# Performance work log

Measured on AMD Instinct MI355X. Metric: run time of the kernel, lower is better.

The kernel has to match this reference:

```python
import jax, jax.numpy as jnp
import numpy as np

T, B, F, H = 2048, 50, 750, 100  # time, batch(seen by LSTM), input feat, hidden
OUT = 2

def setup_inputs() -> dict:
    key = jax.random.key(0)
    ks = jax.random.split(key, 7)
    s = 1.0 / np.sqrt(H)
    u = lambda k, shape: jax.random.uniform(k, shape, jnp.float32, -s, s)
    return {
        "x": jax.random.normal(ks[0], (T, B, F), jnp.float32),
        "W_ih": u(ks[1], (4 * H, F)),
        "W_hh": u(ks[2], (4 * H, H)),
        "b_ih": u(ks[3], (4 * H,)),
        "b_hh": u(ks[4], (4 * H,)),
        "fc_W": u(ks[5], (OUT, B * H)),
        "fc_b": u(ks[6], (OUT,)),
    }

def reference(x, W_ih, W_hh, b_ih, b_hh, fc_W, fc_b):
    # PyTorch LSTM (batch_first=False): scan over dim0. Gate order: i, f, g, o.
    # Precompute input projections for all steps at once: (T, B, 4H)
    x_proj = jnp.einsum('tbf,gf->tbg', x, W_ih) + b_ih + b_hh

    def step(carry, xp):
        h, c = carry                      # (B, H) each
        gates = xp + h @ W_hh.T           # (B, 4H)
        i, f, g, o = jnp.split(gates, 4, axis=-1)
        i = jax.nn.sigmoid(i)
        f = jax.nn.sigmoid(f)
        g = jnp.tanh(g)
        o = jax.nn.sigmoid(o)
        c = f * c + i * g
        h = o * jnp.tanh(c)
        return (h, c), h

    h0 = jnp.zeros((B, H), x.dtype)
    c0 = jnp.zeros((B, H), x.dtype)
    _, hs = jax.lax.scan(step, (h0, c0), x_proj)  # hs: (T, B, H)
    flat = hs.reshape(hs.shape[0], -1)            # (T, B*H) == (T, 5000)
    return flat @ fc_W.T + fc_b                   # (T, 2)
```

## Files before the change

kernel.cpp:

```cpp
#include <hip/hip_runtime.h>

#define T_DIM 2048
#define B_DIM 50
#define F_DIM 750
#define H_DIM 100
#define G4    400
#define M_DIM (T_DIM * B_DIM)
#define KPAD  768

typedef __attribute__((ext_vector_type(8))) short short8v;
typedef __attribute__((ext_vector_type(4))) float f32x4;

__device__ __forceinline__ float fast_rcp(float x) { return __builtin_amdgcn_rcpf(x); }
__device__ __forceinline__ float sigm_f(float x) {
    return fast_rcp(1.0f + __expf(-x));
}
__device__ __forceinline__ float tanh_f(float x) {
    return 1.0f - 2.0f * fast_rcp(__expf(2.0f * x) + 1.0f);
}

__device__ __forceinline__ unsigned short f2bf(float f) {
    unsigned int u = __float_as_uint(f);
    u = (u + 0x7FFFu + ((u >> 16) & 1u)) >> 16;
    return (unsigned short)u;
}
__device__ __forceinline__ float bf2f(unsigned short h) {
    return __uint_as_float(((unsigned int)h) << 16);
}

template <int CTRL>
__device__ __forceinline__ float qperm(float x) {
    return __int_as_float(__builtin_amdgcn_mov_dpp(__float_as_int(x), CTRL, 0xF, 0xF, false));
}

__global__ __launch_bounds__(256) void wconv(
    const float* __restrict__ W,
    unsigned short* __restrict__ Whi,
    unsigned short* __restrict__ Wlo)
{
    int i = blockIdx.x * 256 + threadIdx.x;
    if (i >= G4 * KPAD) return;
    int g = i / KPAD, k = i - g * KPAD;
    float v = (k < F_DIM) ? W[g * F_DIM + k] : 0.f;
    unsigned short h = f2bf(v);
    Whi[i] = h;
    Wlo[i] = f2bf(v - bf2f(h));
}

__global__ __launch_bounds__(256) void xproj_mfma(
    const float* __restrict__ x,
    const unsigned short* __restrict__ Whi,
    const unsigned short* __restrict__ Wlo,
    const float* __restrict__ bih,
    const float* __restrict__ bhh,
    float* __restrict__ xp)
{
    const int m0   = blockIdx.x * 64;
    const int tid  = threadIdx.x;
    const int lane = tid & 63;
    const int w    = tid >> 6;
    const int fr   = lane & 15;
    const int fk   = (lane >> 4) * 8;

    __shared__ unsigned short Ahi[2][64][40];
    __shared__ unsigned short Alo[2][64][40];

    f32x4 acc[4][7];
    #pragma unroll
    for (int s = 0; s < 4; ++s)
        #pragma unroll
        for (int t = 0; t < 7; ++t)
            acc[s][t] = (f32x4){0.f, 0.f, 0.f, 0.f};

    float bias_t[7];
    #pragma unroll
    for (int tt = 0; tt < 7; ++tt) {
        const int nt = w + 4 * tt;
        if (nt < 25) {
            const int n = nt * 16 + fr;
            bias_t[tt] = bih[n] + bhh[n];
        } else bias_t[tt] = 0.f;
    }

    const int sr  = tid >> 2;
    const int sc  = (tid & 3) * 8;
    #define STAGE(KS, NB)                                                        \
    {                                                                            \
        const int kg = (KS) * 32 + sc;                                           \
        const size_t base = (size_t)(m0 + sr) * F_DIM + kg;                      \
        float f[8];                                                              \
        _Pragma("unroll")                                                        \
        for (int i = 0; i < 8; i += 2) {                                         \
            if (kg + i + 1 < F_DIM) {                                            \
                float2 v = *reinterpret_cast<const float2*>(&x[base + i]);       \
                f[i] = v.x; f[i + 1] = v.y;                                      \
            } else {                                                             \
                f[i]     = (kg + i < F_DIM) ? x[base + i] : 0.f;                 \
                f[i + 1] = 0.f;                                                  \
            }                                                                    \
        }                                                                        \
        short8v vh, vl;                                                          \
        _Pragma("unroll")                                                        \
        for (int i = 0; i < 8; ++i) {                                            \
            unsigned short h = f2bf(f[i]);                                       \
            vh[i] = (short)h;                                                    \
            vl[i] = (short)f2bf(f[i] - bf2f(h));                                 \
        }                                                                        \
        *reinterpret_cast<short8v*>(&Ahi[NB][sr][sc]) = vh;                      \
        *reinterpret_cast<short8v*>(&Alo[NB][sr][sc]) = vl;                      \
    }

    STAGE(0, 0);
    asm volatile("s_waitcnt lgkmcnt(0)\ns_barrier" ::: "memory");

    for (int s = 0; s < 24; ++s) {
        const int cur = s & 1;
        short8v ah[4], al[4];
        #pragma unroll
        for (int st = 0; st < 4; ++st) {
            ah[st] = *reinterpret_cast<const short8v*>(&Ahi[cur][st * 16 + fr][fk]);
            al[st] = *reinterpret_cast<const short8v*>(&Alo[cur][st * 16 + fr][fk]);
        }
        if (s + 1 < 24) STAGE(s + 1, cur ^ 1);

        const int kb = s * 32 + fk;
        #pragma unroll
        for (int tt = 0; tt < 7; ++tt) {
            const int nt = w + 4 * tt;
            if (nt < 25) {
                const int n = nt * 16 + fr;
                const short8v bh = *reinterpret_cast<const short8v*>(&Whi[n * KPAD + kb]);
                const short8v bl = *reinterpret_cast<const short8v*>(&Wlo[n * KPAD + kb]);
                #pragma unroll
                for (int st = 0; st < 4; ++st) {
                    acc[st][tt] = __builtin_amdgcn_mfma_f32_16x16x32_bf16(ah[st], bh, acc[st][tt], 0, 0, 0);
                    acc[st][tt] = __builtin_amdgcn_mfma_f32_16x16x32_bf16(ah[st], bl, acc[st][tt], 0, 0, 0);
                    acc[st][tt] = __builtin_amdgcn_mfma_f32_16x16x32_bf16(al[st], bh, acc[st][tt], 0, 0, 0);
                }
            }
        }
        asm volatile("s_waitcnt lgkmcnt(0)\ns_barrier" ::: "memory");
    }

    #pragma unroll
    for (int tt = 0; tt < 7; ++tt) {
        const int nt = w + 4 * tt;
        if (nt < 25) {
            const int n = nt * 16 + fr;
            #pragma unroll
            for (int st = 0; st < 4; ++st) {
                #pragma unroll
                for (int r = 0; r < 4; ++r) {
                    const int m = m0 + st * 16 + (lane >> 4) * 4 + r;
                    xp[(size_t)m * G4 + n] = acc[st][tt][r] + bias_t[tt];
                }
            }
        }
    }
    #undef STAGE
}

__global__ __launch_bounds__(448) void lstm_scan(
    const float* __restrict__ xp,
    const float* __restrict__ Whh,
    float* __restrict__ hs)
{
    const int b   = blockIdx.x;
    const int tid = threadIdx.x;
    const int q   = tid & 3;
    const int j   = tid >> 2;
    const int jc  = (j < H_DIM) ? j : (H_DIM - 1);
    const int row = q * H_DIM + jc;

    __shared__ __align__(16) float hbuf[2][112];

    float w[4][28];
    #pragma unroll
    for (int g = 0; g < 4; ++g) {
        const size_t base = (size_t)(g * H_DIM + jc) * H_DIM + 25 * q;
        #pragma unroll
        for (int r = 0; r < 25; ++r) w[g][r] = Whh[base + r];
        w[g][25] = w[g][26] = w[g][27] = 0.f;
    }
    if (tid < 112) { hbuf[0][tid] = 0.f; hbuf[1][tid] = 0.f; }

    const int hq = jc / 25, hr = jc - (jc / 25) * 25;
    const int hpos = hq * 28 + hr;

    float c = 0.f;
    float xpv = xp[(size_t)b * G4 + row];
    __syncthreads();

    int p = 0;
    for (int t = 0; t < T_DIM; ++t) {
        float xp_next = (t + 1 < T_DIM)
            ? xp[(size_t)((t + 1) * B_DIM + b) * G4 + row] : 0.f;

        float ac[4];
        ac[0] = (q == 0) ? xpv : 0.f;
        ac[1] = (q == 1) ? xpv : 0.f;
        ac[2] = (q == 2) ? xpv : 0.f;
        ac[3] = (q == 3) ? xpv : 0.f;
        #pragma unroll
        for (int k4 = 0; k4 < 7; ++k4) {
            float4 hv = *reinterpret_cast<const float4*>(&hbuf[p][28 * q + 4 * k4]);
            #pragma unroll
            for (int g = 0; g < 4; ++g) {
                ac[g] = fmaf(w[g][4 * k4 + 0], hv.x, ac[g]);
                ac[g] = fmaf(w[g][4 * k4 + 1], hv.y, ac[g]);
                ac[g] = fmaf(w[g][4 * k4 + 2], hv.z, ac[g]);
                ac[g] = fmaf(w[g][4 * k4 + 3], hv.w, ac[g]);
            }
        }
        #pragma unroll
        for (int g = 0; g < 4; ++g) ac[g] += qperm<0xB1>(ac[g]);
        #pragma unroll
        for (int g = 0; g < 4; ++g) ac[g] += qperm<0x4E>(ac[g]);

        const float i_ = sigm_f(ac[0]);
        const float f_ = sigm_f(ac[1]);
        const float g_ = tanh_f(ac[2]);
        const float o_ = sigm_f(ac[3]);
        c = fmaf(f_, c, i_ * g_);
        const float h = o_ * tanh_f(c);

        if (q == 0 && j < H_DIM) {
            hbuf[p ^ 1][hpos] = h;
            hs[(size_t)(t * B_DIM + b) * H_DIM + j] = h;
        }
        asm volatile("s_waitcnt lgkmcnt(0)\ns_barrier" ::: "memory");
        p ^= 1;
        xpv = xp_next;
    }
}

__global__ __launch_bounds__(256) void fc_kernel(
    const float* __restrict__ hs,
    const float* __restrict__ fcW,
    const float* __restrict__ fcb,
    float* __restrict__ out)
{
    const int t   = blockIdx.x;
    const int tid = threadIdx.x;

    float p0 = 0.f, p1 = 0.f;
    for (int k = tid * 4; k < 5000; k += 1024) {
        const float4 hv = *reinterpret_cast<const float4*>(&hs[(size_t)t * 5000 + k]);
        const float4 w0 = *reinterpret_cast<const float4*>(&fcW[k]);
        const float4 w1 = *reinterpret_cast<const float4*>(&fcW[5000 + k]);
        p0 += hv.x * w0.x + hv.y * w0.y + hv.z * w0.z + hv.w * w0.w;
        p1 += hv.x * w1.x + hv.y * w1.y + hv.z * w1.z + hv.w * w1.w;
    }
    #pragma unroll
    for (int off = 32; off > 0; off >>= 1) {
        p0 += __shfl_xor(p0, off);
        p1 += __shfl_xor(p1, off);
    }
    __shared__ float red[8];
    const int wv = tid >> 6;
    if ((tid & 63) == 0) { red[wv * 2] = p0; red[wv * 2 + 1] = p1; }
    __syncthreads();
    if (tid == 0) {
        out[2 * t]     = fcb[0] + red[0] + red[2] + red[4] + red[6];
        out[2 * t + 1] = fcb[1] + red[1] + red[3] + red[5] + red[7];
    }
}

extern "C" void kernel_launch(void* const* d_in, const int* in_sizes, int n_in,
                              void* d_out, int out_size, void* d_ws, size_t ws_size,
                              hipStream_t stream) {
    const float* x   = (const float*)d_in[0];
    const float* Wih = (const float*)d_in[1];
    const float* Whh = (const float*)d_in[2];
    const float* bih = (const float*)d_in[3];
    const float* bhh = (const float*)d_in[4];
    const float* fcW = (const float*)d_in[5];
    const float* fcb = (const float*)d_in[6];
    float* out = (float*)d_out;

    char* ws = (char*)d_ws;
    float*          xp  = (float*)ws;
    unsigned short* Whi = (unsigned short*)(ws + (size_t)M_DIM * G4 * 4);
    unsigned short* Wlo = Whi + (size_t)G4 * KPAD;
    float*          hs  = (float*)((char*)(Wlo + (size_t)G4 * KPAD));

    wconv<<<(G4 * KPAD + 255) / 256, 256, 0, stream>>>(Wih, Whi, Wlo);

    xproj_mfma<<<M_DIM / 64, 256, 0, stream>>>(x, Whi, Wlo, bih, bhh, xp);

    lstm_scan<<<B_DIM, 448, 0, stream>>>(xp, Whh, hs);

    fc_kernel<<<T_DIM, 256, 0, stream>>>(hs, fcW, fcb, out);
}
```

Before: 1.704 ms.

## Truncate bf16 split, defer LDS staging writes, and distribute LSTM gate activations across lanes

The x-projection GEMM now converts activations to hi/lo bf16 by truncation instead of round-to-nearest, and splits staging into a global load before the MFMA loop and an LDS write after it, so load latency overlaps compute. Occupancy hints are added to both kernels. In the recurrent scan, each of the four quad lanes computes one gate activation through a unified sigmoid/tanh formula using exp2, and the results are broadcast with DPP, replacing four transcendental evaluations per lane. Pointer increments replace per-step index arithmetic. Truncation slightly changes the rounding of the split but remains close to fp32 precision.

```diff
diff --git a/kernel.cpp b/kernel.cpp
--- a/kernel.cpp
+++ b/kernel.cpp
@@ -19,7 +19,7 @@
     return 1.0f - 2.0f * fast_rcp(__expf(2.0f * x) + 1.0f);
 }
 
-__device__ __forceinline__ unsigned short f2bf(float f) {
+__device__ __forceinline__ unsigned short f2bf_rne(float f) {
     unsigned int u = __float_as_uint(f);
     u = (u + 0x7FFFu + ((u >> 16) & 1u)) >> 16;
     return (unsigned short)u;
@@ -42,12 +42,12 @@
     if (i >= G4 * KPAD) return;
     int g = i / KPAD, k = i - g * KPAD;
     float v = (k < F_DIM) ? W[g * F_DIM + k] : 0.f;
-    unsigned short h = f2bf(v);
+    unsigned short h = f2bf_rne(v);
     Whi[i] = h;
-    Wlo[i] = f2bf(v - bf2f(h));
-}
-
-__global__ __launch_bounds__(256) void xproj_mfma(
+    Wlo[i] = f2bf_rne(v - bf2f(h));
+}
+
+__global__ __launch_bounds__(256, 2) void xproj_mfma(
     const float* __restrict__ x,
     const unsigned short* __restrict__ Whi,
     const unsigned short* __restrict__ Wlo,
@@ -82,35 +82,43 @@
         } else bias_t[tt] = 0.f;
     }
 
-    const int sr  = tid >> 2;
-    const int sc  = (tid & 3) * 8;
-    #define STAGE(KS, NB)                                                        \
-    {                                                                            \
-        const int kg = (KS) * 32 + sc;                                           \
-        const size_t base = (size_t)(m0 + sr) * F_DIM + kg;                      \
-        float f[8];                                                              \
-        _Pragma("unroll")                                                        \
-        for (int i = 0; i < 8; i += 2) {                                         \
-            if (kg + i + 1 < F_DIM) {                                            \
-                float2 v = *reinterpret_cast<const float2*>(&x[base + i]);       \
-                f[i] = v.x; f[i + 1] = v.y;                                      \
-            } else {                                                             \
-                f[i]     = (kg + i < F_DIM) ? x[base + i] : 0.f;                 \
-                f[i + 1] = 0.f;                                                  \
-            }                                                                    \
-        }                                                                        \
-        short8v vh, vl;                                                          \
-        _Pragma("unroll")                                                        \
-        for (int i = 0; i < 8; ++i) {                                            \
-            unsigned short h = f2bf(f[i]);                                       \
-            vh[i] = (short)h;                                                    \
-            vl[i] = (short)f2bf(f[i] - bf2f(h));                                 \
-        }                                                                        \
-        *reinterpret_cast<short8v*>(&Ahi[NB][sr][sc]) = vh;                      \
-        *reinterpret_cast<short8v*>(&Alo[NB][sr][sc]) = vl;                      \
-    }
-
-    STAGE(0, 0);
+    const int sr = tid >> 2;
+    const int sc = (tid & 3) * 8;
+    const float* xrow = x + (size_t)(m0 + sr) * F_DIM;
+
+    float f[8];
+
+    #define STAGE_LOAD(KS)                                                     \
+    {                                                                          \
+        const int kg = (KS) * 32 + sc;                                         \
+        _Pragma("unroll")                                                      \
+        for (int i = 0; i < 8; i += 2) {                                       \
+            if (kg + i + 1 < F_DIM) {                                          \
+                float2 v = *reinterpret_cast<const float2*>(&xrow[kg + i]);    \
+                f[i] = v.x; f[i + 1] = v.y;                                    \
+            } else {                                                           \
+                f[i]     = (kg + i < F_DIM) ? xrow[kg + i] : 0.f;              \
+                f[i + 1] = 0.f;                                                \
+            }                                                                  \
+        }                                                                      \
+    }
+
+    #define STAGE_WRITE(NB)                                                    \
+    {                                                                          \
+        short8v vh, vl;                                                        \
+        _Pragma("unroll")                                                      \
+        for (int i = 0; i < 8; ++i) {                                          \
+            unsigned int u = __float_as_uint(f[i]);                            \
+            vh[i] = (short)(u >> 16);                                          \
+            float r = f[i] - __uint_as_float(u & 0xffff0000u);                 \
+            vl[i] = (short)(__float_as_uint(r) >> 16);                         \
+        }                                                                      \
+        *reinterpret_cast<short8v*>(&Ahi[NB][sr][sc]) = vh;                    \
+        *reinterpret_cast<short8v*>(&Alo[NB][sr][sc]) = vl;                    \
+    }
+
+    STAGE_LOAD(0);
+    STAGE_WRITE(0);
     asm volatile("s_waitcnt lgkmcnt(0)\ns_barrier" ::: "memory");
 
     for (int s = 0; s < 24; ++s) {
@@ -121,7 +129,8 @@
             ah[st] = *reinterpret_cast<const short8v*>(&Ahi[cur][st * 16 + fr][fk]);
             al[st] = *reinterpret_cast<const short8v*>(&Alo[cur][st * 16 + fr][fk]);
         }
-        if (s + 1 < 24) STAGE(s + 1, cur ^ 1);
+
+        if (s < 23) STAGE_LOAD(s + 1);
 
         const int kb = s * 32 + fk;
         #pragma unroll
@@ -139,6 +148,8 @@
                 }
             }
         }
+
+        if (s < 23) STAGE_WRITE(cur ^ 1);
         asm volatile("s_waitcnt lgkmcnt(0)\ns_barrier" ::: "memory");
     }
 
@@ -157,10 +168,11 @@
             }
         }
     }
-    #undef STAGE
-}
-
-__global__ __launch_bounds__(448) void lstm_scan(
+    #undef STAGE_LOAD
+    #undef STAGE_WRITE
+}
+
+__global__ __launch_bounds__(448, 1) void lstm_scan(
     const float* __restrict__ xp,
     const float* __restrict__ Whh,
     float* __restrict__ hs)
@@ -184,50 +196,79 @@
     }
     if (tid < 112) { hbuf[0][tid] = 0.f; hbuf[1][tid] = 0.f; }
 
-    const int hq = jc / 25, hr = jc - (jc / 25) * 25;
-    const int hpos = hq * 28 + hr;
+    const int hpos = (jc / 25) * 28 + (jc % 25);
+    const bool writer = (q == 0) && (j < H_DIM);
+
+    const float s_act = (q == 2) ? 2.0f : 1.0f;
+    const float nsl2  = -s_act * 1.44269504088896f;
+    const float nsm1  = 1.0f - s_act;
 
     float c = 0.f;
-    float xpv = xp[(size_t)b * G4 + row];
+    const float* xp_ptr = xp + (size_t)b * G4 + row;
+    float*       hs_ptr = hs + (size_t)b * H_DIM + j;
+    float xpv = *xp_ptr;
     __syncthreads();
 
     int p = 0;
     for (int t = 0; t < T_DIM; ++t) {
-        float xp_next = (t + 1 < T_DIM)
-            ? xp[(size_t)((t + 1) * B_DIM + b) * G4 + row] : 0.f;
-
-        float ac[4];
-        ac[0] = (q == 0) ? xpv : 0.f;
-        ac[1] = (q == 1) ? xpv : 0.f;
-        ac[2] = (q == 2) ? xpv : 0.f;
-        ac[3] = (q == 3) ? xpv : 0.f;
+        float xp_next = 0.f;
+        if (t != T_DIM - 1) {
+            xp_ptr += B_DIM * G4;
+            xp_next = *xp_ptr;
+        }
+
+        float ac0 = (q == 0) ? xpv : 0.f;
+        float ac1 = (q == 1) ? xpv : 0.f;
+        float ac2 = (q == 2) ? xpv : 0.f;
+        float ac3 = (q == 3) ? xpv : 0.f;
         #pragma unroll
         for (int k4 = 0; k4 < 7; ++k4) {
             float4 hv = *reinterpret_cast<const float4*>(&hbuf[p][28 * q + 4 * k4]);
-            #pragma unroll
-            for (int g = 0; g < 4; ++g) {
-                ac[g] = fmaf(w[g][4 * k4 + 0], hv.x, ac[g]);
-                ac[g] = fmaf(w[g][4 * k4 + 1], hv.y, ac[g]);
-                ac[g] = fmaf(w[g][4 * k4 + 2], hv.z, ac[g]);
-                ac[g] = fmaf(w[g][4 * k4 + 3], hv.w, ac[g]);
-            }
-        }
-        #pragma unroll
-        for (int g = 0; g < 4; ++g) ac[g] += qperm<0xB1>(ac[g]);
-        #pragma unroll
-        for (int g = 0; g < 4; ++g) ac[g] += qperm<0x4E>(ac[g]);
-
-        const float i_ = sigm_f(ac[0]);
-        const float f_ = sigm_f(ac[1]);
-        const float g_ = tanh_f(ac[2]);
-        const float o_ = sigm_f(ac[3]);
+            ac0 = fmaf(w[0][4 * k4 + 0], hv.x, ac0);
+            ac0 = fmaf(w[0][4 * k4 + 1], hv.y, ac0);
+            ac0 = fmaf(w[0][4 * k4 + 2], hv.z, ac0);
+            ac0 = fmaf(w[0][4 * k4 + 3], hv.w, ac0);
+            ac1 = fmaf(w[1][4 * k4 + 0], hv.x, ac1);
+            ac1 = fmaf(w[1][4 * k4 + 1], hv.y, ac1);
+            ac1 = fmaf(w[1][4 * k4 + 2], hv.z, ac1);
+            ac1 = fmaf(w[1][4 * k4 + 3], hv.w, ac1);
+            ac2 = fmaf(w[2][4 * k4 + 0], hv.x, ac2);
+            ac2 = fmaf(w[2][4 * k4 + 1], hv.y, ac2);
+            ac2 = fmaf(w[2][4 * k4 + 2], hv.z, ac2);
+            ac2 = fmaf(w[2][4 * k4 + 3], hv.w, ac2);
+            ac3 = fmaf(w[3][4 * k4 + 0], hv.x, ac3);
+            ac3 = fmaf(w[3][4 * k4 + 1], hv.y, ac3);
+            ac3 = fmaf(w[3][4 * k4 + 2], hv.z, ac3);
+            ac3 = fmaf(w[3][4 * k4 + 3], hv.w, ac3);
+        }
+        ac0 += qperm<0xB1>(ac0);
+        ac1 += qperm<0xB1>(ac1);
+        ac2 += qperm<0xB1>(ac2);
+        ac3 += qperm<0xB1>(ac3);
+        ac0 += qperm<0x4E>(ac0);
+        ac1 += qperm<0x4E>(ac1);
+        ac2 += qperm<0x4E>(ac2);
+        ac3 += qperm<0x4E>(ac3);
+
+        float pre = ac0;
+        pre = (q == 1) ? ac1 : pre;
+        pre = (q == 2) ? ac2 : pre;
+        pre = (q == 3) ? ac3 : pre;
+        float act = fmaf(s_act, fast_rcp(1.0f + __builtin_amdgcn_exp2f(nsl2 * pre)), nsm1);
+
+        float i_ = qperm<0x00>(act);
+        float f_ = qperm<0x55>(act);
+        float g_ = qperm<0xAA>(act);
+        float o_ = qperm<0xFF>(act);
+
         c = fmaf(f_, c, i_ * g_);
         const float h = o_ * tanh_f(c);
 
-        if (q == 0 && j < H_DIM) {
+        if (writer) {
             hbuf[p ^ 1][hpos] = h;
-            hs[(size_t)(t * B_DIM + b) * H_DIM + j] = h;
-        }
+            *hs_ptr = h;
+        }
+        hs_ptr += B_DIM * H_DIM;
         asm volatile("s_waitcnt lgkmcnt(0)\ns_barrier" ::: "memory");
         p ^= 1;
         xpv = xp_next;
```

Result: faster. 1.493 ms (-12.4%).
